# Kernel optimization log

Measured on AMD Instinct MI355X. Metric: run time of the kernel, lower is better.

The kernel has to match this reference:

```python
import jax, jax.numpy as jnp
import numpy as np

B, N, H, HD = 2, 512, 1024, 512


def setup_inputs() -> dict:
    key = jax.random.key(0)
    ks = jax.random.split(key, 9)
    s = 0.02
    return {
        "emb": jax.random.normal(ks[0], (B, N, H), jnp.float32),
        # start detector: Linear(H->HD), ReLU, Linear(HD->1)
        "W_s1": jax.random.normal(ks[1], (H, HD), jnp.float32) * s,
        "b_s1": jax.random.normal(ks[2], (HD,), jnp.float32) * s,
        "w_s2": jax.random.normal(ks[3], (HD,), jnp.float32) * s,
        "b_s2": jax.random.normal(ks[4], (), jnp.float32) * s,
        # end detector: Linear(2H->HD), ReLU, Linear(HD->1)
        "W_e1": jax.random.normal(ks[5], (2 * H, HD), jnp.float32) * s,
        "b_e1": jax.random.normal(ks[6], (HD,), jnp.float32) * s,
        "w_e2": jax.random.normal(ks[7], (HD,), jnp.float32) * s,
        "b_e2": jax.random.normal(ks[8], (), jnp.float32) * s,
    }


def reference(emb, W_s1, b_s1, w_s2, b_s2, W_e1, b_e1, w_e2, b_e2):
    # start logits: (B, N)
    h_s = jax.nn.relu(jnp.einsum("bnh,hd->bnd", emb, W_s1) + b_s1)
    start_logits = jnp.einsum("bnd,d->bn", h_s, w_s2) + b_s2

    # end logits: math of cat([start_rep, end_rep]) @ W_e1 done as split matmuls
    # (avoids materializing the (B,N,N,2H) concat buffer)
    W1_start, W1_end = W_e1[:H], W_e1[H:]
    a = jnp.einsum("bih,hd->bid", emb, W1_start)  # (B, N, HD) start-token part
    c = jnp.einsum("bjh,hd->bjd", emb, W1_end)    # (B, N, HD) end-token part
    h_e = jax.nn.relu(a[:, :, None, :] + c[:, None, :, :] + b_e1)  # (B, N, N, HD)
    end_logits = jnp.einsum("bijd,d->bij", h_e, w_e2) + b_e2       # (B, N, N)

    return (start_logits, end_logits)
```

## Files before the change

### kernel.cpp

```cpp
#include <hip/hip_runtime.h>
#include <hip/hip_bf16.h>


typedef float f32x4 __attribute__((ext_vector_type(4)));
typedef __bf16 bf16x8 __attribute__((ext_vector_type(8)));

static __device__ __forceinline__ unsigned short f2bf(float f) {
  unsigned int u = __builtin_bit_cast(unsigned int, f);
  u += 0x7FFFu + ((u >> 16) & 1u);
  return (unsigned short)(u >> 16);
}

__global__ __launch_bounds__(256) void prep_emb(
    const float* __restrict__ in, unsigned short* __restrict__ out) {
  int i = (blockIdx.x * 256 + threadIdx.x) * 8;
  float4 v0 = *(const float4*)&in[i];
  float4 v1 = *(const float4*)&in[i + 4];
  ushort4 o0, o1;
  o0.x = f2bf(v0.x); o0.y = f2bf(v0.y); o0.z = f2bf(v0.z); o0.w = f2bf(v0.w);
  o1.x = f2bf(v1.x); o1.y = f2bf(v1.y); o1.z = f2bf(v1.z); o1.w = f2bf(v1.w);
  *(ushort4*)&out[i] = o0;
  *(ushort4*)&out[i + 4] = o1;
}

__global__ __launch_bounds__(256) void transpose_cast2(
    const float* __restrict__ W_s1, const float* __restrict__ W_e1,
    unsigned short* __restrict__ Wt_s, unsigned short* __restrict__ Wt_e) {
  int z = blockIdx.z;
  if (z == 0 && blockIdx.x >= 32) return;
  const float* in = z ? W_e1 : W_s1;
  unsigned short* out = z ? Wt_e : Wt_s;
  int R = z ? 2048 : 1024;
  const int C = 512;
  __shared__ float tile[32][33];
  int r0 = blockIdx.x * 32, c0 = blockIdx.y * 32;
  int t = threadIdx.x;
  int a = t >> 3, b4 = t & 7;
  float4 v = *(const float4*)&in[(size_t)(r0 + a) * C + c0 + b4 * 4];
  tile[a][b4 * 4 + 0] = v.x;
  tile[a][b4 * 4 + 1] = v.y;
  tile[a][b4 * 4 + 2] = v.z;
  tile[a][b4 * 4 + 3] = v.w;
  __syncthreads();
  ushort4 o;
  o.x = f2bf(tile[b4 * 4 + 0][a]);
  o.y = f2bf(tile[b4 * 4 + 1][a]);
  o.z = f2bf(tile[b4 * 4 + 2][a]);
  o.w = f2bf(tile[b4 * 4 + 3][a]);
  *(ushort4*)&out[(size_t)(c0 + a) * R + r0 + b4 * 4] = o;
}

__global__ void init_start_out(float* __restrict__ out,
                               const float* __restrict__ b_s2) {
  float v = b_s2[0];
  int i = threadIdx.x * 4;
  float4 o = {v, v, v, v};
  *(float4*)&out[i] = o;
}

__global__ __launch_bounds__(256) void gemm_fused(
    const unsigned short* __restrict__ Aemb,
    const unsigned short* __restrict__ Wt_s,
    const unsigned short* __restrict__ Wt_e,
    const float* __restrict__ b_s1,
    const float* __restrict__ w_s2,
    const float* __restrict__ b_e1,
    float* __restrict__ out,
    float* __restrict__ A_mat,
    float* __restrict__ C_mat) {
  __shared__ unsigned short Al[64][72];
  __shared__ unsigned short Bl[64][72];
  int z = blockIdx.z;
  int n0 = blockIdx.x * 64;
  int m0 = blockIdx.y * 64;
  const unsigned short* Bmat = (z == 0) ? Wt_s : Wt_e;
  int bstride = (z == 0) ? 1024 : 2048;
  int bofs = (z == 2) ? 1024 : 0;

  int t = threadIdx.x;
  int lane = t & 63, wave = t >> 6;
  int wm = (wave >> 1) * 32, wn = (wave & 1) * 32;
  int lm = lane & 15, g = lane >> 4;

  f32x4 acc[2][2];
#pragma unroll
  for (int mi = 0; mi < 2; ++mi)
#pragma unroll
    for (int ni = 0; ni < 2; ++ni) acc[mi][ni] = (f32x4){0.f, 0.f, 0.f, 0.f};

  int srow = t >> 2, sc = (t & 3) * 16;
  for (int k0 = 0; k0 < 1024; k0 += 64) {
    __syncthreads();
    const unsigned short* ap = &Aemb[(size_t)(m0 + srow) * 1024 + k0 + sc];
    const unsigned short* bp =
        &Bmat[(size_t)(n0 + srow) * bstride + bofs + k0 + sc];
    *(uint4*)&Al[srow][sc] = *(const uint4*)ap;
    *(uint4*)&Al[srow][sc + 8] = *(const uint4*)(ap + 8);
    *(uint4*)&Bl[srow][sc] = *(const uint4*)bp;
    *(uint4*)&Bl[srow][sc + 8] = *(const uint4*)(bp + 8);
    __syncthreads();
#pragma unroll
    for (int kk = 0; kk < 2; ++kk) {
      bf16x8 af[2], bfr[2];
#pragma unroll
      for (int mi = 0; mi < 2; ++mi)
        af[mi] = *(const bf16x8*)&Al[wm + mi * 16 + lm][kk * 32 + g * 8];
#pragma unroll
      for (int ni = 0; ni < 2; ++ni)
        bfr[ni] = *(const bf16x8*)&Bl[wn + ni * 16 + lm][kk * 32 + g * 8];
#pragma unroll
      for (int mi = 0; mi < 2; ++mi)
#pragma unroll
        for (int ni = 0; ni < 2; ++ni)
          acc[mi][ni] = __builtin_amdgcn_mfma_f32_16x16x32_bf16(
              af[mi], bfr[ni], acc[mi][ni], 0, 0, 0);
    }
  }

  if (z == 0) {
    float bs[2], wsv[2];
#pragma unroll
    for (int ni = 0; ni < 2; ++ni) {
      int col = n0 + wn + ni * 16 + lm;
      bs[ni] = b_s1[col];
      wsv[ni] = w_s2[col];
    }
#pragma unroll
    for (int mi = 0; mi < 2; ++mi) {
#pragma unroll
      for (int r = 0; r < 4; ++r) {
        float s = 0.f;
#pragma unroll
        for (int ni = 0; ni < 2; ++ni) {
          float v = acc[mi][ni][r] + bs[ni];
          v = fmaxf(v, 0.f);
          s += v * wsv[ni];
        }
        s += __shfl_xor(s, 1);
        s += __shfl_xor(s, 2);
        s += __shfl_xor(s, 4);
        s += __shfl_xor(s, 8);
        if (lm == 0) {
          int row = m0 + wm + mi * 16 + g * 4 + r;
          atomicAdd(&out[row], s);
        }
      }
    }
  } else {
    float* Out = (z == 1) ? A_mat : C_mat;
    float badd[2];
#pragma unroll
    for (int ni = 0; ni < 2; ++ni) {
      int col = n0 + wn + ni * 16 + lm;
      badd[ni] = (z == 2) ? b_e1[col] : 0.f;
    }
#pragma unroll
    for (int mi = 0; mi < 2; ++mi)
#pragma unroll
      for (int ni = 0; ni < 2; ++ni) {
        int col = n0 + wn + ni * 16 + lm;
#pragma unroll
        for (int r = 0; r < 4; ++r) {
          int row = m0 + wm + mi * 16 + g * 4 + r;
          Out[(size_t)row * 512 + col] = acc[mi][ni][r] + badd[ni];
        }
      }
  }
}

__global__ __launch_bounds__(256) void pairwise(
    const float* __restrict__ A_mat, const float* __restrict__ C_mat,
    const float* __restrict__ w_e2, const float* __restrict__ b_e2,
    float* __restrict__ out) {
  __shared__ float As_t[64][36];
  __shared__ float Cs_t[64][36];
  __shared__ float wl[512];
  int t = threadIdx.x;
  int b = blockIdx.z;
  int j0 = blockIdx.x * 32, i0 = blockIdx.y * 32;

  for (int i = t; i < 512; i += 256) wl[i] = w_e2[i];
  float be2 = b_e2[0];

  int ti = t & 15, tj = t >> 4;
  float accv[2][2] = {{0.f, 0.f}, {0.f, 0.f}};
  const float* Abase = A_mat + (size_t)(b * 512 + i0) * 512;
  const float* Cbase = C_mat + (size_t)(b * 512 + j0) * 512;

  int si = t & 31, sq = t >> 5;
  for (int dc = 0; dc < 512; dc += 64) {
    __syncthreads();
#pragma unroll
    for (int p = 0; p < 2; ++p) {
      int d0 = sq * 4 + p * 32;
      float4 va = *(const float4*)&Abase[(size_t)si * 512 + dc + d0];
      As_t[d0 + 0][si] = va.x;
      As_t[d0 + 1][si] = va.y;
      As_t[d0 + 2][si] = va.z;
      As_t[d0 + 3][si] = va.w;
      float4 vc = *(const float4*)&Cbase[(size_t)si * 512 + dc + d0];
      Cs_t[d0 + 0][si] = vc.x;
      Cs_t[d0 + 1][si] = vc.y;
      Cs_t[d0 + 2][si] = vc.z;
      Cs_t[d0 + 3][si] = vc.w;
    }
    __syncthreads();
#pragma unroll 4
    for (int d = 0; d < 64; ++d) {
      float w = wl[dc + d];
      float2 av = *(const float2*)&As_t[d][ti * 2];
      float2 cv = *(const float2*)&Cs_t[d][tj * 2];
      accv[0][0] += fmaxf(av.x + cv.x, 0.f) * w;
      accv[0][1] += fmaxf(av.x + cv.y, 0.f) * w;
      accv[1][0] += fmaxf(av.y + cv.x, 0.f) * w;
      accv[1][1] += fmaxf(av.y + cv.y, 0.f) * w;
    }
  }

  float* oe = out + 1024;
#pragma unroll
  for (int q = 0; q < 2; ++q) {
    int i = i0 + ti * 2 + q;
    float2 vv;
    vv.x = accv[q][0] + be2;
    vv.y = accv[q][1] + be2;
    *(float2*)&oe[(size_t)(b * 512 + i) * 512 + j0 + tj * 2] = vv;
  }
}

extern "C" void kernel_launch(void* const* d_in, const int* in_sizes, int n_in,
                              void* d_out, int out_size, void* d_ws,
                              size_t ws_size, hipStream_t stream) {
  const float* emb  = (const float*)d_in[0];
  const float* W_s1 = (const float*)d_in[1];
  const float* b_s1 = (const float*)d_in[2];
  const float* w_s2 = (const float*)d_in[3];
  const float* b_s2 = (const float*)d_in[4];
  const float* W_e1 = (const float*)d_in[5];
  const float* b_e1 = (const float*)d_in[6];
  const float* w_e2 = (const float*)d_in[7];
  const float* b_e2 = (const float*)d_in[8];
  float* out = (float*)d_out;

  char* ws = (char*)d_ws;
  unsigned short* emb_bf = (unsigned short*)(ws);
  unsigned short* Wt_s = (unsigned short*)(ws + 2u * (1u << 20));
  unsigned short* Wt_e = (unsigned short*)(ws + 3u * (1u << 20));
  float* A_mat = (float*)(ws + 5u * (1u << 20));
  float* C_mat = (float*)(ws + 7u * (1u << 20));

  hipLaunchKernelGGL(prep_emb, dim3(512), dim3(256), 0, stream, emb, emb_bf);
  hipLaunchKernelGGL(transpose_cast2, dim3(64, 16, 2), dim3(256), 0, stream,
                     W_s1, W_e1, Wt_s, Wt_e);
  hipLaunchKernelGGL(init_start_out, dim3(1), dim3(256), 0, stream, out, b_s2);
  hipLaunchKernelGGL(gemm_fused, dim3(8, 16, 3), dim3(256), 0, stream,
                     emb_bf, Wt_s, Wt_e, b_s1, w_s2, b_e1, out, A_mat, C_mat);
  hipLaunchKernelGGL(pairwise, dim3(16, 16, 2), dim3(256), 0, stream,
                     A_mat, C_mat, w_e2, b_e2, out);
}
```

Before: 129.3 us.

## Merge prep kernels, shrink GEMM tiles, split pairwise over D with packed math

Folds the emb cast, the weight transpose-casts and the output initialisation into one prep launch, which now also pre-fills the end logits with b_e2. The GEMM tile narrows to 64x32 so twice as many blocks run. The pairwise kernel splits the hidden dimension into two halves across blocks, widens each thread to 2x4 outputs, and uses packed float2 add/max/mul. Partial results are combined with atomicAdd into the pre-initialised output. This removes launches and raises parallelism and per-thread ILP, but adds atomic traffic on the large end-logit output and makes the summation order nondeterministic.

```diff
diff --git a/kernel.cpp b/kernel.cpp
--- a/kernel.cpp
+++ b/kernel.cpp
@@ -3,6 +3,7 @@
 
 
 typedef float f32x4 __attribute__((ext_vector_type(4)));
+typedef float f32x2 __attribute__((ext_vector_type(2)));
 typedef __bf16 bf16x8 __attribute__((ext_vector_type(8)));
 
 static __device__ __forceinline__ unsigned short f2bf(float f) {
@@ -11,209 +12,191 @@
   return (unsigned short)(u >> 16);
 }
 
-__global__ __launch_bounds__(256) void prep_emb(
-    const float* __restrict__ in, unsigned short* __restrict__ out) {
-  int i = (blockIdx.x * 256 + threadIdx.x) * 8;
-  float4 v0 = *(const float4*)&in[i];
-  float4 v1 = *(const float4*)&in[i + 4];
-  ushort4 o0, o1;
-  o0.x = f2bf(v0.x); o0.y = f2bf(v0.y); o0.z = f2bf(v0.z); o0.w = f2bf(v0.w);
-  o1.x = f2bf(v1.x); o1.y = f2bf(v1.y); o1.z = f2bf(v1.z); o1.w = f2bf(v1.w);
-  *(ushort4*)&out[i] = o0;
-  *(ushort4*)&out[i + 4] = o1;
-}
-
-__global__ __launch_bounds__(256) void transpose_cast2(
-    const float* __restrict__ W_s1, const float* __restrict__ W_e1,
-    unsigned short* __restrict__ Wt_s, unsigned short* __restrict__ Wt_e) {
-  int z = blockIdx.z;
-  if (z == 0 && blockIdx.x >= 32) return;
-  const float* in = z ? W_e1 : W_s1;
-  unsigned short* out = z ? Wt_e : Wt_s;
-  int R = z ? 2048 : 1024;
-  const int C = 512;
+__global__ __launch_bounds__(256) void prep(
+    const float* __restrict__ emb, const float* __restrict__ W_s1,
+    const float* __restrict__ W_e1, const float* __restrict__ b_s2,
+    const float* __restrict__ b_e2, unsigned short* __restrict__ emb_bf,
+    unsigned short* __restrict__ Wt_s, unsigned short* __restrict__ Wt_e,
+    float* __restrict__ out) {
   __shared__ float tile[32][33];
-  int r0 = blockIdx.x * 32, c0 = blockIdx.y * 32;
-  int t = threadIdx.x;
-  int a = t >> 3, b4 = t & 7;
-  float4 v = *(const float4*)&in[(size_t)(r0 + a) * C + c0 + b4 * 4];
-  tile[a][b4 * 4 + 0] = v.x;
-  tile[a][b4 * 4 + 1] = v.y;
-  tile[a][b4 * 4 + 2] = v.z;
-  tile[a][b4 * 4 + 3] = v.w;
-  __syncthreads();
-  ushort4 o;
-  o.x = f2bf(tile[b4 * 4 + 0][a]);
-  o.y = f2bf(tile[b4 * 4 + 1][a]);
-  o.z = f2bf(tile[b4 * 4 + 2][a]);
-  o.w = f2bf(tile[b4 * 4 + 3][a]);
-  *(ushort4*)&out[(size_t)(c0 + a) * R + r0 + b4 * 4] = o;
-}
-
-__global__ void init_start_out(float* __restrict__ out,
-                               const float* __restrict__ b_s2) {
-  float v = b_s2[0];
-  int i = threadIdx.x * 4;
-  float4 o = {v, v, v, v};
-  *(float4*)&out[i] = o;
+  int bx = blockIdx.x, t = threadIdx.x;
+  if (bx < 512) {
+    int i = bx * 2048 + t * 8;
+    f32x4 v0 = *(const f32x4*)&emb[i];
+    f32x4 v1 = *(const f32x4*)&emb[i + 4];
+    ushort4 o0, o1;
+    o0.x = f2bf(v0[0]); o0.y = f2bf(v0[1]);
+    o0.z = f2bf(v0[2]); o0.w = f2bf(v0[3]);
+    o1.x = f2bf(v1[0]); o1.y = f2bf(v1[1]);
+    o1.z = f2bf(v1[2]); o1.w = f2bf(v1[3]);
+    *(ushort4*)&emb_bf[i] = o0;
+    *(ushort4*)&emb_bf[i + 4] = o1;
+  } else if (bx < 2048) {
+    const float* in;
+    unsigned short* o;
+    int R, tid;
+    if (bx < 1024) { tid = bx - 512;  in = W_s1; o = Wt_s; R = 1024; }
+    else           { tid = bx - 1024; in = W_e1; o = Wt_e; R = 2048; }
+    int r0 = (tid >> 4) * 32, c0 = (tid & 15) * 32;
+    int a = t >> 3, b4 = t & 7;
+    f32x4 v = *(const f32x4*)&in[(size_t)(r0 + a) * 512 + c0 + b4 * 4];
+    tile[a][b4 * 4 + 0] = v[0];
+    tile[a][b4 * 4 + 1] = v[1];
+    tile[a][b4 * 4 + 2] = v[2];
+    tile[a][b4 * 4 + 3] = v[3];
+    __syncthreads();
+    ushort4 o4;
+    o4.x = f2bf(tile[b4 * 4 + 0][a]);
+    o4.y = f2bf(tile[b4 * 4 + 1][a]);
+    o4.z = f2bf(tile[b4 * 4 + 2][a]);
+    o4.w = f2bf(tile[b4 * 4 + 3][a]);
+    *(ushort4*)&o[(size_t)(c0 + a) * R + r0 + b4 * 4] = o4;
+  } else if (bx == 2048) {
+    float v = b_s2[0];
+    f32x4 o = {v, v, v, v};
+    *(f32x4*)&out[t * 4] = o;
+  } else {
+    float v = b_e2[0];
+    f32x4 o = {v, v, v, v};
+    *(f32x4*)&out[1024 + (size_t)(bx - 2049) * 1024 + t * 4] = o;
+  }
 }
 
 __global__ __launch_bounds__(256) void gemm_fused(
     const unsigned short* __restrict__ Aemb,
     const unsigned short* __restrict__ Wt_s,
     const unsigned short* __restrict__ Wt_e,
-    const float* __restrict__ b_s1,
-    const float* __restrict__ w_s2,
-    const float* __restrict__ b_e1,
-    float* __restrict__ out,
-    float* __restrict__ A_mat,
-    float* __restrict__ C_mat) {
+    const float* __restrict__ b_s1, const float* __restrict__ w_s2,
+    const float* __restrict__ b_e1, float* __restrict__ out,
+    float* __restrict__ A_mat, float* __restrict__ C_mat) {
   __shared__ unsigned short Al[64][72];
-  __shared__ unsigned short Bl[64][72];
+  __shared__ unsigned short Bl[32][72];
   int z = blockIdx.z;
-  int n0 = blockIdx.x * 64;
+  int n0 = blockIdx.x * 32;
   int m0 = blockIdx.y * 64;
   const unsigned short* Bmat = (z == 0) ? Wt_s : Wt_e;
   int bstride = (z == 0) ? 1024 : 2048;
   int bofs = (z == 2) ? 1024 : 0;
 
-  int t = threadIdx.x;
-  int lane = t & 63, wave = t >> 6;
-  int wm = (wave >> 1) * 32, wn = (wave & 1) * 32;
+  int t = threadIdx.x, lane = t & 63, wave = t >> 6;
+  int wm = wave * 16;
   int lm = lane & 15, g = lane >> 4;
 
-  f32x4 acc[2][2];
-#pragma unroll
-  for (int mi = 0; mi < 2; ++mi)
-#pragma unroll
-    for (int ni = 0; ni < 2; ++ni) acc[mi][ni] = (f32x4){0.f, 0.f, 0.f, 0.f};
-
-  int srow = t >> 2, sc = (t & 3) * 16;
+  f32x4 acc[2];
+  acc[0] = (f32x4){0.f, 0.f, 0.f, 0.f};
+  acc[1] = (f32x4){0.f, 0.f, 0.f, 0.f};
+
+  int ar = t >> 2, ac = (t & 3) * 16;
+  int br = t >> 3, bc = (t & 7) * 8;
   for (int k0 = 0; k0 < 1024; k0 += 64) {
     __syncthreads();
-    const unsigned short* ap = &Aemb[(size_t)(m0 + srow) * 1024 + k0 + sc];
-    const unsigned short* bp =
-        &Bmat[(size_t)(n0 + srow) * bstride + bofs + k0 + sc];
-    *(uint4*)&Al[srow][sc] = *(const uint4*)ap;
-    *(uint4*)&Al[srow][sc + 8] = *(const uint4*)(ap + 8);
-    *(uint4*)&Bl[srow][sc] = *(const uint4*)bp;
-    *(uint4*)&Bl[srow][sc + 8] = *(const uint4*)(bp + 8);
+    const unsigned short* ap = &Aemb[(size_t)(m0 + ar) * 1024 + k0 + ac];
+    *(uint4*)&Al[ar][ac] = *(const uint4*)ap;
+    *(uint4*)&Al[ar][ac + 8] = *(const uint4*)(ap + 8);
+    *(uint4*)&Bl[br][bc] =
+        *(const uint4*)&Bmat[(size_t)(n0 + br) * bstride + bofs + k0 + bc];
     __syncthreads();
 #pragma unroll
     for (int kk = 0; kk < 2; ++kk) {
-      bf16x8 af[2], bfr[2];
-#pragma unroll
-      for (int mi = 0; mi < 2; ++mi)
-        af[mi] = *(const bf16x8*)&Al[wm + mi * 16 + lm][kk * 32 + g * 8];
-#pragma unroll
-      for (int ni = 0; ni < 2; ++ni)
-        bfr[ni] = *(const bf16x8*)&Bl[wn + ni * 16 + lm][kk * 32 + g * 8];
-#pragma unroll
-      for (int mi = 0; mi < 2; ++mi)
-#pragma unroll
-        for (int ni = 0; ni < 2; ++ni)
-          acc[mi][ni] = __builtin_amdgcn_mfma_f32_16x16x32_bf16(
-              af[mi], bfr[ni], acc[mi][ni], 0, 0, 0);
-    }
-  }
-
+      bf16x8 af = *(const bf16x8*)&Al[wm + lm][kk * 32 + g * 8];
+      bf16x8 b0 = *(const bf16x8*)&Bl[lm][kk * 32 + g * 8];
+      bf16x8 b1 = *(const bf16x8*)&Bl[16 + lm][kk * 32 + g * 8];
+      acc[0] = __builtin_amdgcn_mfma_f32_16x16x32_bf16(af, b0, acc[0], 0, 0, 0);
+      acc[1] = __builtin_amdgcn_mfma_f32_16x16x32_bf16(af, b1, acc[1], 0, 0, 0);
+    }
+  }
+
+  int col0 = n0 + lm, col1 = n0 + 16 + lm;
   if (z == 0) {
-    float bs[2], wsv[2];
-#pragma unroll
-    for (int ni = 0; ni < 2; ++ni) {
-      int col = n0 + wn + ni * 16 + lm;
-      bs[ni] = b_s1[col];
-      wsv[ni] = w_s2[col];
-    }
-#pragma unroll
-    for (int mi = 0; mi < 2; ++mi) {
-#pragma unroll
-      for (int r = 0; r < 4; ++r) {
-        float s = 0.f;
-#pragma unroll
-        for (int ni = 0; ni < 2; ++ni) {
-          float v = acc[mi][ni][r] + bs[ni];
-          v = fmaxf(v, 0.f);
-          s += v * wsv[ni];
-        }
-        s += __shfl_xor(s, 1);
-        s += __shfl_xor(s, 2);
-        s += __shfl_xor(s, 4);
-        s += __shfl_xor(s, 8);
-        if (lm == 0) {
-          int row = m0 + wm + mi * 16 + g * 4 + r;
-          atomicAdd(&out[row], s);
-        }
-      }
+    float bs0 = b_s1[col0], bs1 = b_s1[col1];
+    float ws0 = w_s2[col0], ws1 = w_s2[col1];
+#pragma unroll
+    for (int r = 0; r < 4; ++r) {
+      float s = fmaxf(acc[0][r] + bs0, 0.f) * ws0 +
+                fmaxf(acc[1][r] + bs1, 0.f) * ws1;
+      s += __shfl_xor(s, 1);
+      s += __shfl_xor(s, 2);
+      s += __shfl_xor(s, 4);
+      s += __shfl_xor(s, 8);
+      if (lm == 0) atomicAdd(&out[m0 + wm + g * 4 + r], s);
     }
   } else {
     float* Out = (z == 1) ? A_mat : C_mat;
-    float badd[2];
-#pragma unroll
-    for (int ni = 0; ni < 2; ++ni) {
-      int col = n0 + wn + ni * 16 + lm;
-      badd[ni] = (z == 2) ? b_e1[col] : 0.f;
-    }
-#pragma unroll
-    for (int mi = 0; mi < 2; ++mi)
-#pragma unroll
-      for (int ni = 0; ni < 2; ++ni) {
-        int col = n0 + wn + ni * 16 + lm;
-#pragma unroll
-        for (int r = 0; r < 4; ++r) {
-          int row = m0 + wm + mi * 16 + g * 4 + r;
-          Out[(size_t)row * 512 + col] = acc[mi][ni][r] + badd[ni];
-        }
-      }
+    float b0 = (z == 2) ? b_e1[col0] : 0.f;
+    float b1 = (z == 2) ? b_e1[col1] : 0.f;
+#pragma unroll
+    for (int r = 0; r < 4; ++r) {
+      int row = m0 + wm + g * 4 + r;
+      Out[(size_t)row * 512 + col0] = acc[0][r] + b0;
+      Out[(size_t)row * 512 + col1] = acc[1][r] + b1;
+    }
   }
 }
 
 __global__ __launch_bounds__(256) void pairwise(
     const float* __restrict__ A_mat, const float* __restrict__ C_mat,
-    const float* __restrict__ w_e2, const float* __restrict__ b_e2,
-    float* __restrict__ out) {
-  __shared__ float As_t[64][36];
-  __shared__ float Cs_t[64][36];
-  __shared__ float wl[512];
+    const float* __restrict__ w_e2, float* __restrict__ out) {
+  __shared__ f32x2 As_p[32][32];
+  __shared__ f32x2 Cs_p[32][64];
+  __shared__ f32x2 wlh[128];
   int t = threadIdx.x;
-  int b = blockIdx.z;
-  int j0 = blockIdx.x * 32, i0 = blockIdx.y * 32;
-
-  for (int i = t; i < 512; i += 256) wl[i] = w_e2[i];
-  float be2 = b_e2[0];
+  int b = blockIdx.z >> 1, h = blockIdx.z & 1;
+  int j0 = blockIdx.x * 64, i0 = blockIdx.y * 32;
+  int dbase = h * 256;
+
+  if (t < 128) wlh[t] = *(const f32x2*)&w_e2[dbase + 2 * t];
 
   int ti = t & 15, tj = t >> 4;
-  float accv[2][2] = {{0.f, 0.f}, {0.f, 0.f}};
-  const float* Abase = A_mat + (size_t)(b * 512 + i0) * 512;
-  const float* Cbase = C_mat + (size_t)(b * 512 + j0) * 512;
-
+  f32x2 acc2[2][4];
+#pragma unroll
+  for (int q = 0; q < 2; ++q)
+#pragma unroll
+    for (int r = 0; r < 4; ++r) acc2[q][r] = (f32x2){0.f, 0.f};
+
+  const float* Ab = A_mat + (size_t)(b * 512 + i0) * 512 + dbase;
+  const float* Cb = C_mat + (size_t)(b * 512 + j0) * 512 + dbase;
   int si = t & 31, sq = t >> 5;
-  for (int dc = 0; dc < 512; dc += 64) {
-    __syncthreads();
-#pragma unroll
-    for (int p = 0; p < 2; ++p) {
-      int d0 = sq * 4 + p * 32;
-      float4 va = *(const float4*)&Abase[(size_t)si * 512 + dc + d0];
-      As_t[d0 + 0][si] = va.x;
-      As_t[d0 + 1][si] = va.y;
-      As_t[d0 + 2][si] = va.z;
-      As_t[d0 + 3][si] = va.w;
-      float4 vc = *(const float4*)&Cbase[(size_t)si * 512 + dc + d0];
-      Cs_t[d0 + 0][si] = vc.x;
-      Cs_t[d0 + 1][si] = vc.y;
-      Cs_t[d0 + 2][si] = vc.z;
-      Cs_t[d0 + 3][si] = vc.w;
-    }
-    __syncthreads();
-#pragma unroll 4
-    for (int d = 0; d < 64; ++d) {
-      float w = wl[dc + d];
-      float2 av = *(const float2*)&As_t[d][ti * 2];
-      float2 cv = *(const float2*)&Cs_t[d][tj * 2];
-      accv[0][0] += fmaxf(av.x + cv.x, 0.f) * w;
-      accv[0][1] += fmaxf(av.x + cv.y, 0.f) * w;
-      accv[1][0] += fmaxf(av.y + cv.x, 0.f) * w;
-      accv[1][1] += fmaxf(av.y + cv.y, 0.f) * w;
+  int sj = t & 63, s2 = t >> 6;
+  f32x2 z2 = {0.f, 0.f};
+
+  for (int ch = 0; ch < 4; ++ch) {
+    __syncthreads();
+    {
+      int d0 = sq * 8;
+      f32x4 v0 = *(const f32x4*)&Ab[(size_t)si * 512 + ch * 64 + d0];
+      f32x4 v1 = *(const f32x4*)&Ab[(size_t)si * 512 + ch * 64 + d0 + 4];
+      int dp = d0 >> 1;
+      As_p[dp + 0][si] = (f32x2){v0[0], v0[1]};
+      As_p[dp + 1][si] = (f32x2){v0[2], v0[3]};
+      As_p[dp + 2][si] = (f32x2){v1[0], v1[1]};
+      As_p[dp + 3][si] = (f32x2){v1[2], v1[3]};
+      int e0 = s2 * 16;
+#pragma unroll
+      for (int p = 0; p < 4; ++p) {
+        f32x4 v = *(const f32x4*)&Cb[(size_t)sj * 512 + ch * 64 + e0 + p * 4];
+        int ep = (e0 >> 1) + p * 2;
+        Cs_p[ep + 0][sj] = (f32x2){v[0], v[1]};
+        Cs_p[ep + 1][sj] = (f32x2){v[2], v[3]};
+      }
+    }
+    __syncthreads();
+#pragma unroll 8
+    for (int dp = 0; dp < 32; ++dp) {
+      f32x2 w2 = wlh[ch * 32 + dp];
+      f32x4 av = *(const f32x4*)&As_p[dp][ti * 2];
+      f32x4 cv0 = *(const f32x4*)&Cs_p[dp][tj * 4];
+      f32x4 cv1 = *(const f32x4*)&Cs_p[dp][tj * 4 + 2];
+      f32x2 a0 = {av[0], av[1]}, a1 = {av[2], av[3]};
+      f32x2 c0 = {cv0[0], cv0[1]}, c1 = {cv0[2], cv0[3]};
+      f32x2 c2 = {cv1[0], cv1[1]}, c3 = {cv1[2], cv1[3]};
+      acc2[0][0] += __builtin_elementwise_max(a0 + c0, z2) * w2;
+      acc2[0][1] += __builtin_elementwise_max(a0 + c1, z2) * w2;
+      acc2[0][2] += __builtin_elementwise_max(a0 + c2, z2) * w2;
+      acc2[0][3] += __builtin_elementwise_max(a0 + c3, z2) * w2;
+      acc2[1][0] += __builtin_elementwise_max(a1 + c0, z2) * w2;
+      acc2[1][1] += __builtin_elementwise_max(a1 + c1, z2) * w2;
+      acc2[1][2] += __builtin_elementwise_max(a1 + c2, z2) * w2;
+      acc2[1][3] += __builtin_elementwise_max(a1 + c3, z2) * w2;
     }
   }
 
@@ -221,10 +204,11 @@
 #pragma unroll
   for (int q = 0; q < 2; ++q) {
     int i = i0 + ti * 2 + q;
-    float2 vv;
-    vv.x = accv[q][0] + be2;
-    vv.y = accv[q][1] + be2;
-    *(float2*)&oe[(size_t)(b * 512 + i) * 512 + j0 + tj * 2] = vv;
+#pragma unroll
+    for (int r = 0; r < 4; ++r) {
+      float v = acc2[q][r][0] + acc2[q][r][1];
+      atomicAdd(&oe[(size_t)(b * 512 + i) * 512 + j0 + tj * 4 + r], v);
+    }
   }
 }
 
@@ -249,12 +233,10 @@
   float* A_mat = (float*)(ws + 5u * (1u << 20));
   float* C_mat = (float*)(ws + 7u * (1u << 20));
 
-  hipLaunchKernelGGL(prep_emb, dim3(512), dim3(256), 0, stream, emb, emb_bf);
-  hipLaunchKernelGGL(transpose_cast2, dim3(64, 16, 2), dim3(256), 0, stream,
-                     W_s1, W_e1, Wt_s, Wt_e);
-  hipLaunchKernelGGL(init_start_out, dim3(1), dim3(256), 0, stream, out, b_s2);
-  hipLaunchKernelGGL(gemm_fused, dim3(8, 16, 3), dim3(256), 0, stream,
+  hipLaunchKernelGGL(prep, dim3(2561), dim3(256), 0, stream,
+                     emb, W_s1, W_e1, b_s2, b_e2, emb_bf, Wt_s, Wt_e, out);
+  hipLaunchKernelGGL(gemm_fused, dim3(16, 16, 3), dim3(256), 0, stream,
                      emb_bf, Wt_s, Wt_e, b_s1, w_s2, b_e1, out, A_mat, C_mat);
-  hipLaunchKernelGGL(pairwise, dim3(16, 16, 2), dim3(256), 0, stream,
-                     A_mat, C_mat, w_e2, b_e2, out);
-}
+  hipLaunchKernelGGL(pairwise, dim3(8, 16, 4), dim3(256), 0, stream,
+                     A_mat, C_mat, w_e2, out);
+}
```

New measurement: 123.2 us. -4.7%, faster.
